# Kernel tuning notes

Hardware: AMD Instinct MI355X
Metric: run time of the kernel (lower is better)

The kernel has to match this reference:

```python
import jax, jax.numpy as jnp
import numpy as np

N, D = 12288, 128
T = 0.07  # temperature from __init__ default


def setup_inputs() -> dict:
    key = jax.random.key(0)
    x = jax.random.normal(key, (N, D), dtype=jnp.float32)
    # L2-normalize rows (this loss is defined on unit-norm embeddings;
    # keeps exp(sim / 0.07) finite in fp32 while preserving the exact math).
    x = x / jnp.linalg.norm(x, axis=-1, keepdims=True)
    return {"x": x}


def reference(x):
    # x: [N, D] -> sim: [N, N]
    sim = jnp.matmul(x, x.T) / T
    # faithful to torch: exp -> sum over last dim -> log -> mean (no LSE stabilization)
    return jnp.mean(jnp.log(jnp.sum(jnp.exp(sim), axis=-1)))
```

## Files before the change

kernel.cpp:

```cpp
#include <hip/hip_runtime.h>
#include <hip/hip_bf16.h>

#define NROWS 12288
#define DDIM  128
#define NT    96
#define CHUNK 4
#define NBLK  1200

typedef __bf16 bf16x8 __attribute__((ext_vector_type(8)));
typedef float  f32x4  __attribute__((ext_vector_type(4)));

#define GLD_LDS(g, l) __builtin_amdgcn_global_load_lds(                      \
    (const __attribute__((address_space(1))) void*)(g),                      \
    (__attribute__((address_space(3))) void*)(l), 16, 0, 0)

__device__ __forceinline__ unsigned short f2bf(float f) {
    union { float f; unsigned u; } a; a.f = f;
    unsigned r = a.u + 0x7fffu + ((a.u >> 16) & 1u);
    return (unsigned short)(r >> 16);
}

__global__ void convert_kernel(const float* __restrict__ x, unsigned short* __restrict__ xb,
                               float* __restrict__ rowsum, float* __restrict__ out) {
    int gid = blockIdx.x * 256 + threadIdx.x;
    int i = gid * 4;
    float4 v = *(const float4*)(x + i);
    ushort4 o;
    o.x = f2bf(v.x); o.y = f2bf(v.y); o.z = f2bf(v.z); o.w = f2bf(v.w);
    *(ushort4*)(xb + i) = o;
    if (gid < NROWS) rowsum[gid] = 0.f;
    if (gid == 0) out[0] = 0.f;
}

__device__ __forceinline__ void stage_tile(const unsigned short* __restrict__ xb,
                                           int row0, unsigned short* lds,
                                           int wave, int lane) {
    #pragma unroll
    for (int it = 0; it < 8; ++it) {
        int rbase = wave * 32 + it * 4;
        int r = rbase + (lane >> 4);
        int chunk = (lane & 15) ^ (r & 7);
        GLD_LDS(xb + (size_t)(row0 + r) * DDIM + chunk * 8, lds + rbase * DDIM);
    }
}

__global__ __launch_bounds__(256, 2) void gemm_exp_rowsum(
    const unsigned short* __restrict__ xb, float* __restrict__ rowsum)
{
    __shared__ __align__(16) unsigned short As[128 * DDIM];
    __shared__ __align__(16) unsigned short Bs[128 * DDIM];
    __shared__ float csumS[CHUNK * 128];
    __shared__ float rsum[128];

    const int tid = threadIdx.x;

    int rem = blockIdx.x, bi = 0;
    for (;;) {
        int nch = (NT - bi + CHUNK - 1) / CHUNK;
        if (rem < nch) break;
        rem -= nch; ++bi;
    }
    const int jt0 = bi + rem * CHUNK;
    const int ntiles = min(CHUNK, NT - jt0);
    const int i0 = bi * 128;

    for (int k = tid; k < CHUNK * 128; k += 256) csumS[k] = 0.f;
    if (tid < 128) rsum[tid] = 0.f;

    const int wave = tid >> 6, lane = tid & 63;
    const int wm = wave >> 1, wn = wave & 1;
    const int m16 = lane & 15, q = lane >> 4;

    stage_tile(xb, i0, As, wave, lane);
    __syncthreads();

    bf16x8 af[4][4];
    #pragma unroll
    for (int mi = 0; mi < 4; ++mi) {
        int r = wm * 64 + mi * 16 + m16;
        #pragma unroll
        for (int ks = 0; ks < 4; ++ks)
            af[mi][ks] = *(const bf16x8*)(&As[r * DDIM + (((ks * 4 + q) ^ (r & 7)) * 8)]);
    }

    const float invT = 14.285714285714286f;
    float rp[4][4];
    #pragma unroll
    for (int mi = 0; mi < 4; ++mi)
        #pragma unroll
        for (int r = 0; r < 4; ++r) rp[mi][r] = 0.f;

    for (int t = 0; t < ntiles; ++t) {
        const int jt = jt0 + t;
        __syncthreads();
        stage_tile(xb, jt * 128, Bs, wave, lane);
        __syncthreads();

        f32x4 acc[4][4] = {};
        #pragma unroll
        for (int ks = 0; ks < 4; ++ks) {
            bf16x8 bfr[4];
            #pragma unroll
            for (int ni = 0; ni < 4; ++ni) {
                int r = wn * 64 + ni * 16 + m16;
                bfr[ni] = *(const bf16x8*)(&Bs[r * DDIM + (((ks * 4 + q) ^ (r & 7)) * 8)]);
            }
            #pragma unroll
            for (int mi = 0; mi < 4; ++mi)
                #pragma unroll
                for (int ni = 0; ni < 4; ++ni)
                    acc[mi][ni] = __builtin_amdgcn_mfma_f32_16x16x32_bf16(
                        af[mi][ks], bfr[ni], acc[mi][ni], 0, 0, 0);
        }

        float cp[4] = {0.f, 0.f, 0.f, 0.f};
        #pragma unroll
        for (int mi = 0; mi < 4; ++mi)
            #pragma unroll
            for (int ni = 0; ni < 4; ++ni)
                #pragma unroll
                for (int r = 0; r < 4; ++r) {
                    float ev = __expf(acc[mi][ni][r] * invT);
                    rp[mi][r] += ev;
                    cp[ni] += ev;
                }

        if (jt != bi) {
            #pragma unroll
            for (int ni = 0; ni < 4; ++ni) {
                float s = cp[ni];
                s += __shfl_xor(s, 16);
                s += __shfl_xor(s, 32);
                if (q == 0) atomicAdd(&csumS[t * 128 + wn * 64 + ni * 16 + m16], s);
            }
        }
    }

    #pragma unroll
    for (int mi = 0; mi < 4; ++mi)
        #pragma unroll
        for (int r = 0; r < 4; ++r) {
            float s = rp[mi][r];
            s += __shfl_xor(s, 1);
            s += __shfl_xor(s, 2);
            s += __shfl_xor(s, 4);
            s += __shfl_xor(s, 8);
            if (m16 == 0) atomicAdd(&rsum[wm * 64 + mi * 16 + q * 4 + r], s);
        }
    __syncthreads();

    if (tid < 128) atomicAdd(&rowsum[i0 + tid], rsum[tid]);
    for (int k = tid; k < ntiles * 128; k += 256) {
        float v = csumS[k];
        if (v != 0.f) atomicAdd(&rowsum[jt0 * 128 + k], v);
    }
}

__global__ void finalize_kernel(const float* __restrict__ rowsum, float* __restrict__ out) {
    __shared__ float red[4];
    int gid = blockIdx.x * 256 + threadIdx.x;
    float lg = __logf(rowsum[gid]);
    #pragma unroll
    for (int off = 1; off < 64; off <<= 1)
        lg += __shfl_xor(lg, off);
    const int wv = threadIdx.x >> 6, ln = threadIdx.x & 63;
    if (ln == 0) red[wv] = lg;
    __syncthreads();
    if (threadIdx.x == 0)
        atomicAdd(out, (red[0] + red[1] + red[2] + red[3]) * (1.0f / (float)NROWS));
}

extern "C" void kernel_launch(void* const* d_in, const int* in_sizes, int n_in,
                              void* d_out, int out_size, void* d_ws, size_t ws_size,
                              hipStream_t stream) {
    const float* x = (const float*)d_in[0];
    float* out = (float*)d_out;

    float* rowsum = (float*)d_ws;
    unsigned short* xb = (unsigned short*)((char*)d_ws + NROWS * sizeof(float));

    convert_kernel<<<dim3((NROWS * DDIM) / (4 * 256)), dim3(256), 0, stream>>>(x, xb, rowsum, out);
    gemm_exp_rowsum<<<dim3(NBLK), dim3(256), 0, stream>>>(xb, rowsum);
    finalize_kernel<<<dim3(NROWS / 256), dim3(256), 0, stream>>>(rowsum, out);
}
```

Before: 105.9 us.

## Drop A LDS tile, process B columns in slices, prefetch next tile during exp

Reuses a single LDS buffer for both the A tile load and the B tiles. This halves shared memory and raises the launch bound to 4 blocks per SM. The 4x4 accumulator array is split into column slices so fewer accumulator registers are live at once. The next B tile's global-to-LDS load is issued while the last slice's exponentials are computed, overlapping load with math. exp is replaced by a direct exp2 with the log2e factor folded into the scale constant.

```diff
diff --git a/kernel.cpp b/kernel.cpp
--- a/kernel.cpp
+++ b/kernel.cpp
@@ -44,10 +44,9 @@
     }
 }
 
-__global__ __launch_bounds__(256, 2) void gemm_exp_rowsum(
+__global__ __launch_bounds__(256, 4) void gemm_exp_rowsum(
     const unsigned short* __restrict__ xb, float* __restrict__ rowsum)
 {
-    __shared__ __align__(16) unsigned short As[128 * DDIM];
     __shared__ __align__(16) unsigned short Bs[128 * DDIM];
     __shared__ float csumS[CHUNK * 128];
     __shared__ float rsum[128];
@@ -71,7 +70,7 @@
     const int wm = wave >> 1, wn = wave & 1;
     const int m16 = lane & 15, q = lane >> 4;
 
-    stage_tile(xb, i0, As, wave, lane);
+    stage_tile(xb, i0, Bs, wave, lane);
     __syncthreads();
 
     bf16x8 af[4][4];
@@ -80,10 +79,13 @@
         int r = wm * 64 + mi * 16 + m16;
         #pragma unroll
         for (int ks = 0; ks < 4; ++ks)
-            af[mi][ks] = *(const bf16x8*)(&As[r * DDIM + (((ks * 4 + q) ^ (r & 7)) * 8)]);
-    }
-
-    const float invT = 14.285714285714286f;
+            af[mi][ks] = *(const bf16x8*)(&Bs[r * DDIM + (((ks * 4 + q) ^ (r & 7)) * 8)]);
+    }
+    __syncthreads();
+
+    stage_tile(xb, jt0 * 128, Bs, wave, lane);
+
+    const float C = 20.609929155556624f;
     float rp[4][4];
     #pragma unroll
     for (int mi = 0; mi < 4; ++mi)
@@ -92,47 +94,62 @@
 
     for (int t = 0; t < ntiles; ++t) {
         const int jt = jt0 + t;
+        const bool offd = (jt != bi);
         __syncthreads();
-        stage_tile(xb, jt * 128, Bs, wave, lane);
+
+        f32x4 accL[4];
+        float cpL = 0.f;
+
+        #pragma unroll
+        for (int p = 0; p < 4; ++p) {
+            const int br = wn * 64 + p * 16 + m16;
+            const int bbase = br * DDIM;
+            const int bsw = br & 7;
+
+            f32x4 acc[4] = {};
+            #pragma unroll
+            for (int ks = 0; ks < 4; ++ks) {
+                bf16x8 b = *(const bf16x8*)(&Bs[bbase + (((ks * 4 + q) ^ bsw) * 8)]);
+                #pragma unroll
+                for (int mi = 0; mi < 4; ++mi)
+                    acc[mi] = __builtin_amdgcn_mfma_f32_16x16x32_bf16(af[mi][ks], b, acc[mi], 0, 0, 0);
+            }
+
+            if (p < 3) {
+                float cp = 0.f;
+                #pragma unroll
+                for (int mi = 0; mi < 4; ++mi)
+                    #pragma unroll
+                    for (int r = 0; r < 4; ++r) {
+                        float ev = __builtin_amdgcn_exp2f(acc[mi][r] * C);
+                        rp[mi][r] += ev;
+                        cp += ev;
+                    }
+                cp += __shfl_xor(cp, 16);
+                cp += __shfl_xor(cp, 32);
+                if (offd && q == 0) atomicAdd(&csumS[t * 128 + wn * 64 + p * 16 + m16], cp);
+            } else {
+                #pragma unroll
+                for (int mi = 0; mi < 4; ++mi) accL[mi] = acc[mi];
+            }
+        }
+
         __syncthreads();
-
-        f32x4 acc[4][4] = {};
-        #pragma unroll
-        for (int ks = 0; ks < 4; ++ks) {
-            bf16x8 bfr[4];
-            #pragma unroll
-            for (int ni = 0; ni < 4; ++ni) {
-                int r = wn * 64 + ni * 16 + m16;
-                bfr[ni] = *(const bf16x8*)(&Bs[r * DDIM + (((ks * 4 + q) ^ (r & 7)) * 8)]);
-            }
+        if (t + 1 < ntiles) stage_tile(xb, (jt + 1) * 128, Bs, wave, lane);
+
+        {
+            float cp = 0.f;
             #pragma unroll
             for (int mi = 0; mi < 4; ++mi)
                 #pragma unroll
-                for (int ni = 0; ni < 4; ++ni)
-                    acc[mi][ni] = __builtin_amdgcn_mfma_f32_16x16x32_bf16(
-                        af[mi][ks], bfr[ni], acc[mi][ni], 0, 0, 0);
-        }
-
-        float cp[4] = {0.f, 0.f, 0.f, 0.f};
-        #pragma unroll
-        for (int mi = 0; mi < 4; ++mi)
-            #pragma unroll
-            for (int ni = 0; ni < 4; ++ni)
-                #pragma unroll
                 for (int r = 0; r < 4; ++r) {
-                    float ev = __expf(acc[mi][ni][r] * invT);
+                    float ev = __builtin_amdgcn_exp2f(accL[mi][r] * C);
                     rp[mi][r] += ev;
-                    cp[ni] += ev;
+                    cp += ev;
                 }
-
-        if (jt != bi) {
-            #pragma unroll
-            for (int ni = 0; ni < 4; ++ni) {
-                float s = cp[ni];
-                s += __shfl_xor(s, 16);
-                s += __shfl_xor(s, 32);
-                if (q == 0) atomicAdd(&csumS[t * 128 + wn * 64 + ni * 16 + m16], s);
-            }
+            cp += __shfl_xor(cp, 16);
+            cp += __shfl_xor(cp, 32);
+            if (offd && q == 0) atomicAdd(&csumS[t * 128 + wn * 64 + 3 * 16 + m16], cp);
         }
     }
 
```

New measurement: 222.6 us. +110.2%, slower.

## Double-buffer B tiles, use exp2 intrinsic, fuse finalize via last-block counter

Applied to the files above, without the earlier changes.

The GEMM kernel now double-buffers the B tile in LDS, reusing the A staging buffer, so the next tile's global-to-LDS load overlaps the current tile's MFMA and exp work. There is one barrier per iteration instead of two. The exp is computed as a raw exp2 with the 1/T·log2e constant folded in. The separate finalize launch is removed: a global atomic counter picks the last block, which computes the log-mean itself, saving a kernel launch at the cost of a serial tail done by one block.

```diff
diff --git a/kernel.cpp b/kernel.cpp
--- a/kernel.cpp
+++ b/kernel.cpp
@@ -21,7 +21,8 @@
 }
 
 __global__ void convert_kernel(const float* __restrict__ x, unsigned short* __restrict__ xb,
-                               float* __restrict__ rowsum, float* __restrict__ out) {
+                               float* __restrict__ rowsum, unsigned* __restrict__ counter,
+                               float* __restrict__ out) {
     int gid = blockIdx.x * 256 + threadIdx.x;
     int i = gid * 4;
     float4 v = *(const float4*)(x + i);
@@ -29,7 +30,7 @@
     o.x = f2bf(v.x); o.y = f2bf(v.y); o.z = f2bf(v.z); o.w = f2bf(v.w);
     *(ushort4*)(xb + i) = o;
     if (gid < NROWS) rowsum[gid] = 0.f;
-    if (gid == 0) out[0] = 0.f;
+    if (gid == 0) { out[0] = 0.f; *counter = 0u; }
 }
 
 __device__ __forceinline__ void stage_tile(const unsigned short* __restrict__ xb,
@@ -45,12 +46,14 @@
 }
 
 __global__ __launch_bounds__(256, 2) void gemm_exp_rowsum(
-    const unsigned short* __restrict__ xb, float* __restrict__ rowsum)
+    const unsigned short* __restrict__ xb, float* __restrict__ rowsum,
+    unsigned* __restrict__ counter, float* __restrict__ out)
 {
-    __shared__ __align__(16) unsigned short As[128 * DDIM];
-    __shared__ __align__(16) unsigned short Bs[128 * DDIM];
+    __shared__ __align__(16) unsigned short Bs0[128 * DDIM];
+    __shared__ __align__(16) unsigned short Bs1[128 * DDIM];
     __shared__ float csumS[CHUNK * 128];
     __shared__ float rsum[128];
+    __shared__ unsigned doneS;
 
     const int tid = threadIdx.x;
 
@@ -71,7 +74,7 @@
     const int wm = wave >> 1, wn = wave & 1;
     const int m16 = lane & 15, q = lane >> 4;
 
-    stage_tile(xb, i0, As, wave, lane);
+    stage_tile(xb, i0, Bs0, wave, lane);
     __syncthreads();
 
     bf16x8 af[4][4];
@@ -80,21 +83,23 @@
         int r = wm * 64 + mi * 16 + m16;
         #pragma unroll
         for (int ks = 0; ks < 4; ++ks)
-            af[mi][ks] = *(const bf16x8*)(&As[r * DDIM + (((ks * 4 + q) ^ (r & 7)) * 8)]);
+            af[mi][ks] = *(const bf16x8*)(&Bs0[r * DDIM + (((ks * 4 + q) ^ (r & 7)) * 8)]);
     }
+    stage_tile(xb, jt0 * 128, Bs1, wave, lane);
+    __syncthreads();
 
-    const float invT = 14.285714285714286f;
+    const float C = 20.609929155556624f;
     float rp[4][4];
     #pragma unroll
     for (int mi = 0; mi < 4; ++mi)
         #pragma unroll
         for (int r = 0; r < 4; ++r) rp[mi][r] = 0.f;
 
+    const unsigned short* cur = Bs1;
+    unsigned short* nxt = Bs0;
+
     for (int t = 0; t < ntiles; ++t) {
-        const int jt = jt0 + t;
-        __syncthreads();
-        stage_tile(xb, jt * 128, Bs, wave, lane);
-        __syncthreads();
+        if (t + 1 < ntiles) stage_tile(xb, (jt0 + t + 1) * 128, nxt, wave, lane);
 
         f32x4 acc[4][4] = {};
         #pragma unroll
@@ -103,7 +108,7 @@
             #pragma unroll
             for (int ni = 0; ni < 4; ++ni) {
                 int r = wn * 64 + ni * 16 + m16;
-                bfr[ni] = *(const bf16x8*)(&Bs[r * DDIM + (((ks * 4 + q) ^ (r & 7)) * 8)]);
+                bfr[ni] = *(const bf16x8*)(&cur[r * DDIM + (((ks * 4 + q) ^ (r & 7)) * 8)]);
             }
             #pragma unroll
             for (int mi = 0; mi < 4; ++mi)
@@ -120,12 +125,12 @@
             for (int ni = 0; ni < 4; ++ni)
                 #pragma unroll
                 for (int r = 0; r < 4; ++r) {
-                    float ev = __expf(acc[mi][ni][r] * invT);
+                    float ev = __builtin_amdgcn_exp2f(acc[mi][ni][r] * C);
                     rp[mi][r] += ev;
                     cp[ni] += ev;
                 }
 
-        if (jt != bi) {
+        if (jt0 + t != bi) {
             #pragma unroll
             for (int ni = 0; ni < 4; ++ni) {
                 float s = cp[ni];
@@ -134,6 +139,9 @@
                 if (q == 0) atomicAdd(&csumS[t * 128 + wn * 64 + ni * 16 + m16], s);
             }
         }
+
+        __syncthreads();
+        const unsigned short* tswap = cur; cur = nxt; nxt = (unsigned short*)tswap;
     }
 
     #pragma unroll
@@ -154,20 +162,25 @@
         float v = csumS[k];
         if (v != 0.f) atomicAdd(&rowsum[jt0 * 128 + k], v);
     }
-}
 
-__global__ void finalize_kernel(const float* __restrict__ rowsum, float* __restrict__ out) {
-    __shared__ float red[4];
-    int gid = blockIdx.x * 256 + threadIdx.x;
-    float lg = __logf(rowsum[gid]);
-    #pragma unroll
-    for (int off = 1; off < 64; off <<= 1)
-        lg += __shfl_xor(lg, off);
-    const int wv = threadIdx.x >> 6, ln = threadIdx.x & 63;
-    if (ln == 0) red[wv] = lg;
     __syncthreads();
-    if (threadIdx.x == 0)
-        atomicAdd(out, (red[0] + red[1] + red[2] + red[3]) * (1.0f / (float)NROWS));
+    if (tid == 0) {
+        __threadfence();
+        doneS = atomicAdd(counter, 1u);
+    }
+    __syncthreads();
+    if (doneS == NBLK - 1) {
+        float a = 0.f;
+        for (int i = tid; i < NROWS; i += 256)
+            a += __logf(atomicAdd(&rowsum[i], 0.0f));
+        #pragma unroll
+        for (int off = 1; off < 64; off <<= 1)
+            a += __shfl_xor(a, off);
+        if (lane == 0) rsum[wave] = a;
+        __syncthreads();
+        if (tid == 0)
+            out[0] = (rsum[0] + rsum[1] + rsum[2] + rsum[3]) * (1.0f / (float)NROWS);
+    }
 }
 
 extern "C" void kernel_launch(void* const* d_in, const int* in_sizes, int n_in,
@@ -177,9 +190,9 @@
     float* out = (float*)d_out;
 
     float* rowsum = (float*)d_ws;
-    unsigned short* xb = (unsigned short*)((char*)d_ws + NROWS * sizeof(float));
+    unsigned* counter = (unsigned*)((char*)d_ws + NROWS * sizeof(float));
+    unsigned short* xb = (unsigned short*)((char*)d_ws + NROWS * sizeof(float) + 256);
 
-    convert_kernel<<<dim3((NROWS * DDIM) / (4 * 256)), dim3(256), 0, stream>>>(x, xb, rowsum, out);
-    gemm_exp_rowsum<<<dim3(NBLK), dim3(256), 0, stream>>>(xb, rowsum);
-    finalize_kernel<<<dim3(NROWS / 256), dim3(256), 0, stream>>>(rowsum, out);
+    convert_kernel<<<dim3((NROWS * DDIM) / (4 * 256)), dim3(256), 0, stream>>>(x, xb, rowsum, counter, out);
+    gemm_exp_rowsum<<<dim3(NBLK), dim3(256), 0, stream>>>(xb, rowsum, counter, out);
 }
```

After: 126.8 us. +19.7%, slower.
